# Kernel tuning notes

Hardware: AMD Instinct MI355X
Metric: run time of the kernel (lower is better)

## Reference

```python
import jax, jax.numpy as jnp
import numpy as np
import math

D_MODEL = 1024
NUM_HEADS = 16
HEAD_DIM = D_MODEL // NUM_HEADS


def setup_inputs() -> dict:
    key = jax.random.key(0)
    ks = jax.random.split(key, 9)
    B, T = 4, 2048
    s = 1.0 / math.sqrt(D_MODEL)
    return {
        "x": jax.random.normal(ks[0], (B, T, D_MODEL), dtype=jnp.float32),
        "Wq": jax.random.normal(ks[1], (D_MODEL, D_MODEL), dtype=jnp.float32) * s,
        "bq": jnp.zeros((D_MODEL,), dtype=jnp.float32),
        "Wk": jax.random.normal(ks[2], (D_MODEL, D_MODEL), dtype=jnp.float32) * s,
        "bk": jnp.zeros((D_MODEL,), dtype=jnp.float32),
        "Wv": jax.random.normal(ks[3], (D_MODEL, D_MODEL), dtype=jnp.float32) * s,
        "bv": jnp.zeros((D_MODEL,), dtype=jnp.float32),
        "Wo": jax.random.normal(ks[4], (D_MODEL, D_MODEL), dtype=jnp.float32) * s,
        "bo": jnp.zeros((D_MODEL,), dtype=jnp.float32),
    }


def reference(x, Wq, bq, Wk, bk, Wv, bv, Wo, bo):
    # x: [B, T, D]. Weights stored as [in, out] (torch Linear weight transposed).
    B, T, D = x.shape
    H, Hd = NUM_HEADS, HEAD_DIM

    def heads(w, b):
        # [B,T,D] -> [B,H,T,Hd]
        return (x @ w + b).reshape(B, T, H, Hd).transpose(0, 2, 1, 3)

    q = heads(Wq, bq)
    k = heads(Wk, bk)
    v = heads(Wv, bv)

    scores = jnp.einsum("bhqd,bhkd->bhqk", q, k) / math.sqrt(Hd)
    attn = jax.nn.softmax(scores, axis=-1)  # dropout is identity in eval mode
    ctx = jnp.einsum("bhqk,bhkd->bhqd", attn, v)
    ctx = ctx.transpose(0, 2, 1, 3).reshape(B, T, D)
    return ctx @ Wo + bo
```

## Files before the change

kernel.cpp:

```cpp
#include <hip/hip_runtime.h>
#include <hip/hip_bf16.h>

#define D_MODEL 1024
#define NHEADS  16
#define HD      64
#define BATCH   4
#define SEQ     2048
#define MROWS   (BATCH*SEQ)
#define NKV     (SEQ/64)

typedef __attribute__((ext_vector_type(8))) short bf16x8;
typedef __attribute__((ext_vector_type(4))) float f32x4;
typedef __attribute__((ext_vector_type(16))) float f32x16;
typedef __attribute__((ext_vector_type(2))) float f32x2;
typedef __attribute__((ext_vector_type(4))) unsigned int u32x4;
typedef __attribute__((ext_vector_type(2))) unsigned int u32x2;
#define MFMA16(a,b,c) __builtin_amdgcn_mfma_f32_16x16x32_bf16(a,b,c,0,0,0)
#define MFMA32(a,b,c) __builtin_amdgcn_mfma_f32_32x32x16_bf16(a,b,c,0,0,0)

__device__ __forceinline__ short f2bf(float f) {
    __hip_bfloat16 h = __float2bfloat16(f);
    return *reinterpret_cast<short*>(&h);
}
__device__ __forceinline__ unsigned cvtpk(float a, float b) {
    unsigned r; asm("v_cvt_pk_bf16_f32 %0, %1, %2" : "=v"(r) : "v"(a), "v"(b)); return r;
}
__device__ __forceinline__ float fexp2(float x) {
    float r; asm("v_exp_f32 %0, %1" : "=v"(r) : "v"(x)); return r;
}
__device__ __forceinline__ f32x2 pkadd(f32x2 a, f32x2 b) {
    f32x2 d; asm("v_pk_add_f32 %0, %1, %2" : "=v"(d) : "v"(a), "v"(b)); return d;
}
#define SH2(V,I) __builtin_shufflevector(V, V, I, (I)+1)

typedef const __attribute__((address_space(1))) unsigned char* gas_t;
typedef __attribute__((address_space(3))) unsigned char* las_t;
#define GLD16(gp, lp) __builtin_amdgcn_global_load_lds((gas_t)(gp), (las_t)(lp), 16, 0, 0)

__global__ __launch_bounds__(256) void prep(
    const float* __restrict__ x,
    const float* __restrict__ Wq, const float* __restrict__ Wk,
    const float* __restrict__ Wv, const float* __restrict__ Wo,
    short* __restrict__ xb,
    short* __restrict__ WqT, short* __restrict__ WkT,
    short* __restrict__ WvT, short* __restrict__ WoT)
{
    __shared__ float tile[64][65];
    const int bid = blockIdx.x;
    const int t = threadIdx.x;
    if (bid < 4096) {
        const size_t i = ((size_t)bid * 256 + t) * 8;
        float4 a = *reinterpret_cast<const float4*>(&x[i]);
        float4 b = *reinterpret_cast<const float4*>(&x[i + 4]);
        bf16x8 v;
        v[0]=f2bf(a.x); v[1]=f2bf(a.y); v[2]=f2bf(a.z); v[3]=f2bf(a.w);
        v[4]=f2bf(b.x); v[5]=f2bf(b.y); v[6]=f2bf(b.z); v[7]=f2bf(b.w);
        *reinterpret_cast<bf16x8*>(&xb[i]) = v;
        return;
    }
    const int tt = bid - 4096;
    const int w = tt >> 8;
    const int tl = tt & 255;
    const int bn = (tl & 15) * 64, bk = (tl >> 4) * 64;
    const float* W = (w==0)?Wq:(w==1)?Wk:(w==2)?Wv:Wo;
    short* out     = (w==0)?WqT:(w==1)?WkT:(w==2)?WvT:WoT;
    const int r = t >> 2, c0 = (t & 3) * 16;
    #pragma unroll
    for (int i = 0; i < 16; i += 4) {
        float4 v = *reinterpret_cast<const float4*>(&W[(size_t)(bk + r) * D_MODEL + bn + c0 + i]);
        tile[r][c0+i] = v.x; tile[r][c0+i+1] = v.y; tile[r][c0+i+2] = v.z; tile[r][c0+i+3] = v.w;
    }
    __syncthreads();
    bf16x8 H0, H1;
    #pragma unroll
    for (int i = 0; i < 8; i++) { H0[i] = f2bf(tile[c0 + i][r]); H1[i] = f2bf(tile[c0 + 8 + i][r]); }
    short* hp = &out[(size_t)(bn + r) * D_MODEL + bk + c0];
    *reinterpret_cast<bf16x8*>(hp) = H0;
    *reinterpret_cast<bf16x8*>(hp + 8) = H1;
}

__global__ __launch_bounds__(256) void gemm_qkv(
    const short* __restrict__ A,
    const short* __restrict__ WqT, const short* __restrict__ WkT, const short* __restrict__ WvT,
    const float* __restrict__ bq, const float* __restrict__ bk, const float* __restrict__ bv,
    short* __restrict__ qo, short* __restrict__ ko, short* __restrict__ vo,
    const float qscale)
{
    __shared__ short As[2][128 * 32];
    __shared__ short Bs[2][128 * 32];
    const int tid = threadIdx.x, wave = tid >> 6, lane = tid & 63;
    const int g = lane >> 4, li = lane & 15;
    const int lin = blockIdx.x + blockIdx.y * 24;
    const int swz = (lin & 7) * 192 + (lin >> 3);
    const int bx = swz % 24, by = swz / 24;
    const int which = bx >> 3;
    const int bm = by * 128, bn = (bx & 7) * 128;
    const int wr = wave >> 1, wc = wave & 1;
    const int lrow = lane >> 2, lcol = (lane & 3) * 8;

    const short* BT = (which == 0) ? WqT : (which == 1) ? WkT : WvT;
    const float* bias = (which == 0) ? bq : (which == 1) ? bk : bv;
    short* out = (which == 0) ? qo : (which == 1) ? ko : vo;
    const float scale = (which == 0) ? qscale : 1.0f;

    f32x4 acc[4][4];
    #pragma unroll
    for (int i = 0; i < 4; i++)
        #pragma unroll
        for (int j = 0; j < 4; j++)
            #pragma unroll
            for (int r = 0; r < 4; r++) acc[i][j][r] = 0.f;

#define STAGEG(KS, BUF) do { \
        const int k0_ = (KS) * 32; \
        _Pragma("unroll") \
        for (int c = 0; c < 2; c++) { \
            const int ch = wave + c * 4; \
            const int row = ch * 16 + lrow; \
            GLD16(&A [(size_t)(bm + row) * D_MODEL + k0_ + lcol], &As[BUF][ch * 512]); \
            GLD16(&BT[(size_t)(bn + row) * D_MODEL + k0_ + lcol], &Bs[BUF][ch * 512]); \
        } \
    } while (0)

    STAGEG(0, 0);

    const int NSTEP = D_MODEL / 32;
    for (int ks = 0; ks < NSTEP; ks++) {
        const int cur = ks & 1;
        if (ks + 1 < NSTEP) {
            STAGEG(ks + 1, cur ^ 1);
            asm volatile("s_waitcnt vmcnt(4)" ::: "memory");
        } else {
            asm volatile("s_waitcnt vmcnt(0)" ::: "memory");
        }
        __builtin_amdgcn_s_barrier();
        __builtin_amdgcn_sched_barrier(0);

        bf16x8 af[4], bfr[4];
        #pragma unroll
        for (int mi = 0; mi < 4; mi++) af[mi]  = *reinterpret_cast<const bf16x8*>(&As[cur][(wr * 64 + mi * 16 + li) * 32 + g * 8]);
        #pragma unroll
        for (int ni = 0; ni < 4; ni++) bfr[ni] = *reinterpret_cast<const bf16x8*>(&Bs[cur][(wc * 64 + ni * 16 + li) * 32 + g * 8]);
        #pragma unroll
        for (int mi = 0; mi < 4; mi++)
            #pragma unroll
            for (int ni = 0; ni < 4; ni++)
                acc[mi][ni] = MFMA16(af[mi], bfr[ni], acc[mi][ni]);
        __builtin_amdgcn_s_barrier();
    }
#undef STAGEG

    #pragma unroll
    for (int mi = 0; mi < 4; mi++) {
        #pragma unroll
        for (int r = 0; r < 4; r++) {
            const int m = bm + wr * 64 + mi * 16 + g * 4 + r;
            const int b = m >> 11, t = m & (SEQ - 1);
            #pragma unroll
            for (int ni = 0; ni < 4; ni++) {
                const int n = bn + wc * 64 + ni * 16 + li;
                const float val = (acc[mi][ni][r] + bias[n]) * scale;
                const int h = n >> 6, hd = n & 63;
                const int bh = b * NHEADS + h;
                const short sv = f2bf(val);
                if (which == 0) {
                    out[((size_t)bh * SEQ + t) * HD + hd] = sv;
                } else if (which == 1) {
                    const int kt = t >> 6, trow = t & 63;
                    const int rh = trow >> 5, rl = trow & 31;
                    const int dc = hd >> 4, hh = (hd >> 3) & 1, j = hd & 7;
                    out[((((size_t)bh * NKV + kt) * 8 + dc * 2 + rh) * 64 + hh * 32 + rl) * 8 + j] = sv;
                } else {
                    const int kt = t >> 6, trow = t & 63;
                    const int kb2 = trow >> 4, hh = (trow >> 3) & 1, j = trow & 7;
                    const int vh = hd >> 5, rl = hd & 31;
                    out[((((size_t)bh * NKV + kt) * 8 + kb2 * 2 + vh) * 64 + hh * 32 + rl) * 8 + j] = sv;
                }
            }
        }
    }
}

__global__ __launch_bounds__(256) void gemm_wo(
    const short* __restrict__ A, const short* __restrict__ BT,
    const float* __restrict__ bias, float* __restrict__ out)
{
    __shared__ short As[3][128 * 32];
    __shared__ short Bs[3][128 * 32];
    const int tid = threadIdx.x, wave = tid >> 6, lane = tid & 63;
    const int g = lane >> 4, li = lane & 15;
    const int lin = blockIdx.x + blockIdx.y * 8;
    const int swz = (lin & 7) * 64 + (lin >> 3);
    const int bm = (swz >> 3) * 128, bn = (swz & 7) * 128;
    const int wr = wave >> 1, wc = wave & 1;
    const int lrow = lane >> 2, lcol = (lane & 3) * 8;

    f32x4 acc[4][4];
    #pragma unroll
    for (int i = 0; i < 4; i++)
        #pragma unroll
        for (int j = 0; j < 4; j++)
            #pragma unroll
            for (int r = 0; r < 4; r++) acc[i][j][r] = 0.f;

#define STAGEG(KS, BUF) do { \
        const int k0_ = (KS) * 32; \
        _Pragma("unroll") \
        for (int c = 0; c < 2; c++) { \
            const int ch = wave + c * 4; \
            const int row = ch * 16 + lrow; \
            GLD16(&A [(size_t)(bm + row) * D_MODEL + k0_ + lcol], &As[BUF][ch * 512]); \
            GLD16(&BT[(size_t)(bn + row) * D_MODEL + k0_ + lcol], &Bs[BUF][ch * 512]); \
        } \
    } while (0)

    STAGEG(0, 0);
    STAGEG(1, 1);

    const int NSTEP = D_MODEL / 32;
    for (int ks = 0; ks < NSTEP; ks++) {
        const int cur = ks % 3;
        if (ks + 2 < NSTEP) {
            STAGEG(ks + 2, (ks + 2) % 3);
            asm volatile("s_waitcnt vmcnt(8)" ::: "memory");
        } else if (ks + 1 < NSTEP) {
            asm volatile("s_waitcnt vmcnt(4)" ::: "memory");
        } else {
            asm volatile("s_waitcnt vmcnt(0)" ::: "memory");
        }
        __builtin_amdgcn_s_barrier();
        __builtin_amdgcn_sched_barrier(0);

        bf16x8 af[4], bfr[4];
        #pragma unroll
        for (int mi = 0; mi < 4; mi++) af[mi]  = *reinterpret_cast<const bf16x8*>(&As[cur][(wr * 64 + mi * 16 + li) * 32 + g * 8]);
        #pragma unroll
        for (int ni = 0; ni < 4; ni++) bfr[ni] = *reinterpret_cast<const bf16x8*>(&Bs[cur][(wc * 64 + ni * 16 + li) * 32 + g * 8]);
        #pragma unroll
        for (int mi = 0; mi < 4; mi++)
            #pragma unroll
            for (int ni = 0; ni < 4; ni++)
                acc[mi][ni] = MFMA16(af[mi], bfr[ni], acc[mi][ni]);
        __builtin_amdgcn_s_barrier();
    }
#undef STAGEG

    #pragma unroll
    for (int mi = 0; mi < 4; mi++) {
        #pragma unroll
        for (int r = 0; r < 4; r++) {
            const int m = bm + wr * 64 + mi * 16 + g * 4 + r;
            #pragma unroll
            for (int ni = 0; ni < 4; ni++) {
                const int n = bn + wc * 64 + ni * 16 + li;
                out[(size_t)m * D_MODEL + n] = acc[mi][ni][r] + bias[n];
            }
        }
    }
}

__global__ __launch_bounds__(256) void attn_mfma(
    const short* __restrict__ q, const short* __restrict__ kblk,
    const short* __restrict__ vblk, short* __restrict__ ch)
{
    __shared__ short Ks[2][64 * 64];
    __shared__ short Vs[2][64 * 64];

    const int bh = blockIdx.x;
    const int b  = bh >> 4, h = bh & (NHEADS - 1);
    const int qt = blockIdx.y;
    const int tid = threadIdx.x;
    const int wave = tid >> 6, lane = tid & 63;
    const int ql = lane & 31;
    const int hi = lane >> 5;
    const int lb = lane * 8;

    const short* qp = q + ((size_t)bh * SEQ + qt * 128 + wave * 32 + ql) * HD;
    const bf16x8 qf0 = *reinterpret_cast<const bf16x8*>(qp + 0  + hi * 8);
    const bf16x8 qf1 = *reinterpret_cast<const bf16x8*>(qp + 16 + hi * 8);
    const bf16x8 qf2 = *reinterpret_cast<const bf16x8*>(qp + 32 + hi * 8);
    const bf16x8 qf3 = *reinterpret_cast<const bf16x8*>(qp + 48 + hi * 8);

    f32x16 o0, o1, Z;
    #pragma unroll
    for (int i = 0; i < 16; i++) { o0[i] = 0.f; o1[i] = 0.f; Z[i] = 0.f; }
    float lR = 0.f;

    const int r0 = wave * 2, r1 = wave * 2 + 1;

#define STAGE(T, BUF) do { \
        const short* kg_ = kblk + ((size_t)(bh * NKV + (T)) * 8) * 512; \
        const short* vg_ = vblk + ((size_t)(bh * NKV + (T)) * 8) * 512; \
        GLD16(kg_ + r0 * 512 + lb, &Ks[BUF][r0 * 512]); \
        GLD16(kg_ + r1 * 512 + lb, &Ks[BUF][r1 * 512]); \
        GLD16(vg_ + r0 * 512 + lb, &Vs[BUF][r0 * 512]); \
        GLD16(vg_ + r1 * 512 + lb, &Vs[BUF][r1 * 512]); \
    } while (0)

    u32x4 pp[4];
    bf16x8 vr0[4], vr1[4];

    STAGE(0, 0);

    const int NT = NKV;
    for (int kt = 0; kt < NT; kt++) {
        const int cur = kt & 1;
        if (kt + 1 < NT) {
            STAGE(kt + 1, cur ^ 1);
            asm volatile("s_waitcnt vmcnt(4)" ::: "memory");
        } else {
            asm volatile("s_waitcnt vmcnt(0)" ::: "memory");
        }
        __builtin_amdgcn_s_barrier();
        __builtin_amdgcn_sched_barrier(0);

        const short* Kb = Ks[cur];
        const short* Vb = Vs[cur];

        f32x16 s0, s1;
        __builtin_amdgcn_s_setprio(1);
#define QK_STEP(DC, QF, C0, C1) do { \
            const bf16x8 ka0 = *reinterpret_cast<const bf16x8*>(&Kb[((DC) * 2 + 0) * 512 + lb]); \
            const bf16x8 ka1 = *reinterpret_cast<const bf16x8*>(&Kb[((DC) * 2 + 1) * 512 + lb]); \
            s0 = MFMA32(ka0, QF, C0); \
            s1 = MFMA32(ka1, QF, C1); \
        } while (0)
        QK_STEP(0, qf0, Z, Z);
        QK_STEP(1, qf1, s0, s1);
        QK_STEP(2, qf2, s0, s1);
        QK_STEP(3, qf3, s0, s1);
#undef QK_STEP

        if (kt > 0) {
            #pragma unroll
            for (int KB = 0; KB < 4; KB++) {
                const bf16x8 pf = __builtin_bit_cast(bf16x8, pp[KB]);
                o0 = MFMA32(vr0[KB], pf, o0);
                o1 = MFMA32(vr1[KB], pf, o1);
            }
        }
        #pragma unroll
        for (int KB = 0; KB < 4; KB++) {
            vr0[KB] = *reinterpret_cast<const bf16x8*>(&Vb[(KB * 2 + 0) * 512 + lb]);
            vr1[KB] = *reinterpret_cast<const bf16x8*>(&Vb[(KB * 2 + 1) * 512 + lb]);
        }
        __builtin_amdgcn_s_setprio(0);

        #pragma unroll
        for (int i = 0; i < 16; i++) s0[i] = fexp2(s0[i]);
        #pragma unroll
        for (int i = 0; i < 16; i++) s1[i] = fexp2(s1[i]);
        {
            f32x2 p0 = pkadd(SH2(s0, 0), SH2(s0, 2));
            f32x2 p1 = pkadd(SH2(s0, 4), SH2(s0, 6));
            f32x2 p2 = pkadd(SH2(s0, 8), SH2(s0, 10));
            f32x2 p3 = pkadd(SH2(s0, 12), SH2(s0, 14));
            f32x2 p4 = pkadd(SH2(s1, 0), SH2(s1, 2));
            f32x2 p5 = pkadd(SH2(s1, 4), SH2(s1, 6));
            f32x2 p6 = pkadd(SH2(s1, 8), SH2(s1, 10));
            f32x2 p7 = pkadd(SH2(s1, 12), SH2(s1, 14));
            p0 = pkadd(p0, p1); p2 = pkadd(p2, p3);
            p4 = pkadd(p4, p5); p6 = pkadd(p6, p7);
            p0 = pkadd(p0, p2); p4 = pkadd(p4, p6);
            p0 = pkadd(p0, p4);
            float sum = p0[0] + p0[1];
            sum += __shfl_xor(sum, 32);
            lR += sum;
        }

#define PACK(KB, SS, B) do { \
            const unsigned a0 = cvtpk(SS[(B) + 0], SS[(B) + 1]); \
            const unsigned a1 = cvtpk(SS[(B) + 2], SS[(B) + 3]); \
            const unsigned a2 = cvtpk(SS[(B) + 4], SS[(B) + 5]); \
            const unsigned a3 = cvtpk(SS[(B) + 6], SS[(B) + 7]); \
            const u32x2 r02 = __builtin_amdgcn_permlane32_swap(a0, a2, false, false); \
            const u32x2 r13 = __builtin_amdgcn_permlane32_swap(a1, a3, false, false); \
            pp[KB][0] = r02[0]; pp[KB][1] = r13[0]; pp[KB][2] = r02[1]; pp[KB][3] = r13[1]; \
        } while (0)
        PACK(0, s0, 0); PACK(1, s0, 8); PACK(2, s1, 0); PACK(3, s1, 8);
#undef PACK

        asm volatile("s_waitcnt lgkmcnt(0)" ::: "memory");
        __builtin_amdgcn_sched_barrier(0);
        __builtin_amdgcn_s_barrier();
    }
#undef STAGE

    #pragma unroll
    for (int KB = 0; KB < 4; KB++) {
        const bf16x8 pf = __builtin_bit_cast(bf16x8, pp[KB]);
        o0 = MFMA32(vr0[KB], pf, o0);
        o1 = MFMA32(vr1[KB], pf, o1);
    }

    const float inv = 1.0f / lR;
    const int t = qt * 128 + wave * 32 + ql;
    const size_t base = ((size_t)(b * SEQ + t)) * D_MODEL + h * HD;
    #pragma unroll
    for (int blk = 0; blk < 4; blk++) {
        uint2 w0, w1;
        w0.x = cvtpk(o0[4*blk + 0] * inv, o0[4*blk + 1] * inv);
        w0.y = cvtpk(o0[4*blk + 2] * inv, o0[4*blk + 3] * inv);
        w1.x = cvtpk(o1[4*blk + 0] * inv, o1[4*blk + 1] * inv);
        w1.y = cvtpk(o1[4*blk + 2] * inv, o1[4*blk + 3] * inv);
        *reinterpret_cast<uint2*>(&ch[base + 8*blk + 4*hi])      = w0;
        *reinterpret_cast<uint2*>(&ch[base + 32 + 8*blk + 4*hi]) = w1;
    }
}

extern "C" void kernel_launch(void* const* d_in, const int* in_sizes, int n_in,
                              void* d_out, int out_size, void* d_ws, size_t ws_size,
                              hipStream_t stream) {
    const float* x  = (const float*)d_in[0];
    const float* Wq = (const float*)d_in[1];
    const float* bq = (const float*)d_in[2];
    const float* Wk = (const float*)d_in[3];
    const float* bk = (const float*)d_in[4];
    const float* Wv = (const float*)d_in[5];
    const float* bv = (const float*)d_in[6];
    const float* Wo = (const float*)d_in[7];
    const float* bo = (const float*)d_in[8];

    const size_t S1 = (size_t)MROWS * D_MODEL;
    const size_t SW = (size_t)D_MODEL * D_MODEL;
    short* xb  = (short*)d_ws;
    short* qb  = xb + S1;
    short* kb  = qb + S1;
    short* vb  = kb + S1;
    short* chb = vb + S1;
    short* WqT = chb + S1;
    short* WkT = WqT + SW;
    short* WvT = WkT + SW;
    short* WoT = WvT + SW;

    prep<<<5120, 256, 0, stream>>>(x, Wq, Wk, Wv, Wo, xb, WqT, WkT, WvT, WoT);

    const float QSCALE = 0.125f * 1.4426950408889634f;
    gemm_qkv<<<dim3(24, 64), 256, 0, stream>>>(xb, WqT, WkT, WvT, bq, bk, bv,
                                               qb, kb, vb, QSCALE);
    attn_mfma<<<dim3(BATCH * NHEADS, SEQ / 128), 256, 0, stream>>>(qb, kb, vb, chb);
    gemm_wo<<<dim3(8, 64), 256, 0, stream>>>(chb, WoT, bo, (float*)d_out);
}
```

Measured before the change: 203.9 us.

## Double per-wave query rows in attention and triple-buffer QKV GEMM loads

The attention kernel now gives each wave two 32-row query groups (256 rows per block), so every K/V tile staged into shared memory is reused by twice as many queries. This halves the K/V traffic per query and halves the grid. The P·V step is no longer deferred to the next iteration; it runs right after each half's exp and sum, so one half's softmax can interleave with the other's MFMAs. The QKV GEMM moves from a two-stage to a three-stage LDS pipeline so loads are issued two steps ahead. The costs are more registers and fewer blocks (occupancy, a 512-block grid on many CUs), plus more shared memory in the GEMM.

```diff
diff --git a/kernel.cpp b/kernel.cpp
--- a/kernel.cpp
+++ b/kernel.cpp
@@ -86,8 +86,8 @@
     short* __restrict__ qo, short* __restrict__ ko, short* __restrict__ vo,
     const float qscale)
 {
-    __shared__ short As[2][128 * 32];
-    __shared__ short Bs[2][128 * 32];
+    __shared__ short As[3][128 * 32];
+    __shared__ short Bs[3][128 * 32];
     const int tid = threadIdx.x, wave = tid >> 6, lane = tid & 63;
     const int g = lane >> 4, li = lane & 15;
     const int lin = blockIdx.x + blockIdx.y * 24;
@@ -123,12 +123,15 @@
     } while (0)
 
     STAGEG(0, 0);
+    STAGEG(1, 1);
 
     const int NSTEP = D_MODEL / 32;
     for (int ks = 0; ks < NSTEP; ks++) {
-        const int cur = ks & 1;
-        if (ks + 1 < NSTEP) {
-            STAGEG(ks + 1, cur ^ 1);
+        const int cur = ks % 3;
+        if (ks + 2 < NSTEP) {
+            STAGEG(ks + 2, (ks + 2) % 3);
+            asm volatile("s_waitcnt vmcnt(8)" ::: "memory");
+        } else if (ks + 1 < NSTEP) {
             asm volatile("s_waitcnt vmcnt(4)" ::: "memory");
         } else {
             asm volatile("s_waitcnt vmcnt(0)" ::: "memory");
@@ -275,16 +278,19 @@
     const int hi = lane >> 5;
     const int lb = lane * 8;
 
-    const short* qp = q + ((size_t)bh * SEQ + qt * 128 + wave * 32 + ql) * HD;
-    const bf16x8 qf0 = *reinterpret_cast<const bf16x8*>(qp + 0  + hi * 8);
-    const bf16x8 qf1 = *reinterpret_cast<const bf16x8*>(qp + 16 + hi * 8);
-    const bf16x8 qf2 = *reinterpret_cast<const bf16x8*>(qp + 32 + hi * 8);
-    const bf16x8 qf3 = *reinterpret_cast<const bf16x8*>(qp + 48 + hi * 8);
-
-    f32x16 o0, o1, Z;
-    #pragma unroll
-    for (int i = 0; i < 16; i++) { o0[i] = 0.f; o1[i] = 0.f; Z[i] = 0.f; }
-    float lR = 0.f;
+    const short* qpA = q + ((size_t)bh * SEQ + qt * 256 + wave * 64 + ql) * HD;
+    const short* qpB = qpA + 32 * HD;
+    bf16x8 qfA[4], qfB[4];
+    #pragma unroll
+    for (int dc = 0; dc < 4; dc++) {
+        qfA[dc] = *reinterpret_cast<const bf16x8*>(qpA + dc * 16 + hi * 8);
+        qfB[dc] = *reinterpret_cast<const bf16x8*>(qpB + dc * 16 + hi * 8);
+    }
+
+    f32x16 oA0, oA1, oB0, oB1, Z;
+    #pragma unroll
+    for (int i = 0; i < 16; i++) { oA0[i] = 0.f; oA1[i] = 0.f; oB0[i] = 0.f; oB1[i] = 0.f; Z[i] = 0.f; }
+    float lRA = 0.f, lRB = 0.f;
 
     const int r0 = wave * 2, r1 = wave * 2 + 1;
 
@@ -297,9 +303,6 @@
         GLD16(vg_ + r1 * 512 + lb, &Vs[BUF][r1 * 512]); \
     } while (0)
 
-    u32x4 pp[4];
-    bf16x8 vr0[4], vr1[4];
-
     STAGE(0, 0);
 
     const int NT = NKV;
@@ -317,68 +320,93 @@
         const short* Kb = Ks[cur];
         const short* Vb = Vs[cur];
 
-        f32x16 s0, s1;
+        f32x16 sA0, sA1, sB0, sB1;
         __builtin_amdgcn_s_setprio(1);
-#define QK_STEP(DC, QF, C0, C1) do { \
+#define QK_STEP(DC, CA0, CA1, CB0, CB1) do { \
             const bf16x8 ka0 = *reinterpret_cast<const bf16x8*>(&Kb[((DC) * 2 + 0) * 512 + lb]); \
             const bf16x8 ka1 = *reinterpret_cast<const bf16x8*>(&Kb[((DC) * 2 + 1) * 512 + lb]); \
-            s0 = MFMA32(ka0, QF, C0); \
-            s1 = MFMA32(ka1, QF, C1); \
+            sA0 = MFMA32(ka0, qfA[DC], CA0); \
+            sA1 = MFMA32(ka1, qfA[DC], CA1); \
+            sB0 = MFMA32(ka0, qfB[DC], CB0); \
+            sB1 = MFMA32(ka1, qfB[DC], CB1); \
         } while (0)
-        QK_STEP(0, qf0, Z, Z);
-        QK_STEP(1, qf1, s0, s1);
-        QK_STEP(2, qf2, s0, s1);
-        QK_STEP(3, qf3, s0, s1);
+        QK_STEP(0, Z, Z, Z, Z);
+        QK_STEP(1, sA0, sA1, sB0, sB1);
+        QK_STEP(2, sA0, sA1, sB0, sB1);
+        QK_STEP(3, sA0, sA1, sB0, sB1);
 #undef QK_STEP
-
-        if (kt > 0) {
-            #pragma unroll
-            for (int KB = 0; KB < 4; KB++) {
-                const bf16x8 pf = __builtin_bit_cast(bf16x8, pp[KB]);
-                o0 = MFMA32(vr0[KB], pf, o0);
-                o1 = MFMA32(vr1[KB], pf, o1);
-            }
-        }
-        #pragma unroll
-        for (int KB = 0; KB < 4; KB++) {
-            vr0[KB] = *reinterpret_cast<const bf16x8*>(&Vb[(KB * 2 + 0) * 512 + lb]);
-            vr1[KB] = *reinterpret_cast<const bf16x8*>(&Vb[(KB * 2 + 1) * 512 + lb]);
-        }
         __builtin_amdgcn_s_setprio(0);
 
-        #pragma unroll
-        for (int i = 0; i < 16; i++) s0[i] = fexp2(s0[i]);
-        #pragma unroll
-        for (int i = 0; i < 16; i++) s1[i] = fexp2(s1[i]);
+        bf16x8 vf[8];
+        #pragma unroll
+        for (int rr = 0; rr < 8; rr++)
+            vf[rr] = *reinterpret_cast<const bf16x8*>(&Vb[rr * 512 + lb]);
+
+        #pragma unroll
+        for (int i = 0; i < 16; i++) sA0[i] = fexp2(sA0[i]);
+        #pragma unroll
+        for (int i = 0; i < 16; i++) sA1[i] = fexp2(sA1[i]);
         {
-            f32x2 p0 = pkadd(SH2(s0, 0), SH2(s0, 2));
-            f32x2 p1 = pkadd(SH2(s0, 4), SH2(s0, 6));
-            f32x2 p2 = pkadd(SH2(s0, 8), SH2(s0, 10));
-            f32x2 p3 = pkadd(SH2(s0, 12), SH2(s0, 14));
-            f32x2 p4 = pkadd(SH2(s1, 0), SH2(s1, 2));
-            f32x2 p5 = pkadd(SH2(s1, 4), SH2(s1, 6));
-            f32x2 p6 = pkadd(SH2(s1, 8), SH2(s1, 10));
-            f32x2 p7 = pkadd(SH2(s1, 12), SH2(s1, 14));
+            f32x2 p0 = pkadd(SH2(sA0, 0), SH2(sA0, 2));
+            f32x2 p1 = pkadd(SH2(sA0, 4), SH2(sA0, 6));
+            f32x2 p2 = pkadd(SH2(sA0, 8), SH2(sA0, 10));
+            f32x2 p3 = pkadd(SH2(sA0, 12), SH2(sA0, 14));
+            f32x2 p4 = pkadd(SH2(sA1, 0), SH2(sA1, 2));
+            f32x2 p5 = pkadd(SH2(sA1, 4), SH2(sA1, 6));
+            f32x2 p6 = pkadd(SH2(sA1, 8), SH2(sA1, 10));
+            f32x2 p7 = pkadd(SH2(sA1, 12), SH2(sA1, 14));
             p0 = pkadd(p0, p1); p2 = pkadd(p2, p3);
             p4 = pkadd(p4, p5); p6 = pkadd(p6, p7);
             p0 = pkadd(p0, p2); p4 = pkadd(p4, p6);
             p0 = pkadd(p0, p4);
             float sum = p0[0] + p0[1];
             sum += __shfl_xor(sum, 32);
-            lR += sum;
-        }
-
-#define PACK(KB, SS, B) do { \
+            lRA += sum;
+        }
+        __builtin_amdgcn_s_setprio(1);
+#define PV_STEP(KB, SS, B, O0, O1) do { \
             const unsigned a0 = cvtpk(SS[(B) + 0], SS[(B) + 1]); \
             const unsigned a1 = cvtpk(SS[(B) + 2], SS[(B) + 3]); \
             const unsigned a2 = cvtpk(SS[(B) + 4], SS[(B) + 5]); \
             const unsigned a3 = cvtpk(SS[(B) + 6], SS[(B) + 7]); \
             const u32x2 r02 = __builtin_amdgcn_permlane32_swap(a0, a2, false, false); \
             const u32x2 r13 = __builtin_amdgcn_permlane32_swap(a1, a3, false, false); \
-            pp[KB][0] = r02[0]; pp[KB][1] = r13[0]; pp[KB][2] = r02[1]; pp[KB][3] = r13[1]; \
+            u32x4 wv; \
+            wv[0] = r02[0]; wv[1] = r13[0]; wv[2] = r02[1]; wv[3] = r13[1]; \
+            const bf16x8 pf = __builtin_bit_cast(bf16x8, wv); \
+            O0 = MFMA32(vf[(KB) * 2 + 0], pf, O0); \
+            O1 = MFMA32(vf[(KB) * 2 + 1], pf, O1); \
         } while (0)
-        PACK(0, s0, 0); PACK(1, s0, 8); PACK(2, s1, 0); PACK(3, s1, 8);
-#undef PACK
+        PV_STEP(0, sA0, 0, oA0, oA1); PV_STEP(1, sA0, 8, oA0, oA1);
+        PV_STEP(2, sA1, 0, oA0, oA1); PV_STEP(3, sA1, 8, oA0, oA1);
+        __builtin_amdgcn_s_setprio(0);
+
+        #pragma unroll
+        for (int i = 0; i < 16; i++) sB0[i] = fexp2(sB0[i]);
+        #pragma unroll
+        for (int i = 0; i < 16; i++) sB1[i] = fexp2(sB1[i]);
+        {
+            f32x2 p0 = pkadd(SH2(sB0, 0), SH2(sB0, 2));
+            f32x2 p1 = pkadd(SH2(sB0, 4), SH2(sB0, 6));
+            f32x2 p2 = pkadd(SH2(sB0, 8), SH2(sB0, 10));
+            f32x2 p3 = pkadd(SH2(sB0, 12), SH2(sB0, 14));
+            f32x2 p4 = pkadd(SH2(sB1, 0), SH2(sB1, 2));
+            f32x2 p5 = pkadd(SH2(sB1, 4), SH2(sB1, 6));
+            f32x2 p6 = pkadd(SH2(sB1, 8), SH2(sB1, 10));
+            f32x2 p7 = pkadd(SH2(sB1, 12), SH2(sB1, 14));
+            p0 = pkadd(p0, p1); p2 = pkadd(p2, p3);
+            p4 = pkadd(p4, p5); p6 = pkadd(p6, p7);
+            p0 = pkadd(p0, p2); p4 = pkadd(p4, p6);
+            p0 = pkadd(p0, p4);
+            float sum = p0[0] + p0[1];
+            sum += __shfl_xor(sum, 32);
+            lRB += sum;
+        }
+        __builtin_amdgcn_s_setprio(1);
+        PV_STEP(0, sB0, 0, oB0, oB1); PV_STEP(1, sB0, 8, oB0, oB1);
+        PV_STEP(2, sB1, 0, oB0, oB1); PV_STEP(3, sB1, 8, oB0, oB1);
+#undef PV_STEP
+        __builtin_amdgcn_s_setprio(0);
 
         asm volatile("s_waitcnt lgkmcnt(0)" ::: "memory");
         __builtin_amdgcn_sched_barrier(0);
@@ -386,25 +414,26 @@
     }
 #undef STAGE
 
-    #pragma unroll
-    for (int KB = 0; KB < 4; KB++) {
-        const bf16x8 pf = __builtin_bit_cast(bf16x8, pp[KB]);
-        o0 = MFMA32(vr0[KB], pf, o0);
-        o1 = MFMA32(vr1[KB], pf, o1);
-    }
-
-    const float inv = 1.0f / lR;
-    const int t = qt * 128 + wave * 32 + ql;
-    const size_t base = ((size_t)(b * SEQ + t)) * D_MODEL + h * HD;
+    const int tA = qt * 256 + wave * 64 + ql;
+    const float invA = 1.0f / lRA;
+    const size_t baseA = ((size_t)(b * SEQ + tA)) * D_MODEL + h * HD;
+    const float invB = 1.0f / lRB;
+    const size_t baseB = ((size_t)(b * SEQ + tA + 32)) * D_MODEL + h * HD;
     #pragma unroll
     for (int blk = 0; blk < 4; blk++) {
         uint2 w0, w1;
-        w0.x = cvtpk(o0[4*blk + 0] * inv, o0[4*blk + 1] * inv);
-        w0.y = cvtpk(o0[4*blk + 2] * inv, o0[4*blk + 3] * inv);
-        w1.x = cvtpk(o1[4*blk + 0] * inv, o1[4*blk + 1] * inv);
-        w1.y = cvtpk(o1[4*blk + 2] * inv, o1[4*blk + 3] * inv);
-        *reinterpret_cast<uint2*>(&ch[base + 8*blk + 4*hi])      = w0;
-        *reinterpret_cast<uint2*>(&ch[base + 32 + 8*blk + 4*hi]) = w1;
+        w0.x = cvtpk(oA0[4*blk + 0] * invA, oA0[4*blk + 1] * invA);
+        w0.y = cvtpk(oA0[4*blk + 2] * invA, oA0[4*blk + 3] * invA);
+        w1.x = cvtpk(oA1[4*blk + 0] * invA, oA1[4*blk + 1] * invA);
+        w1.y = cvtpk(oA1[4*blk + 2] * invA, oA1[4*blk + 3] * invA);
+        *reinterpret_cast<uint2*>(&ch[baseA + 8*blk + 4*hi])      = w0;
+        *reinterpret_cast<uint2*>(&ch[baseA + 32 + 8*blk + 4*hi]) = w1;
+        w0.x = cvtpk(oB0[4*blk + 0] * invB, oB0[4*blk + 1] * invB);
+        w0.y = cvtpk(oB0[4*blk + 2] * invB, oB0[4*blk + 3] * invB);
+        w1.x = cvtpk(oB1[4*blk + 0] * invB, oB1[4*blk + 1] * invB);
+        w1.y = cvtpk(oB1[4*blk + 2] * invB, oB1[4*blk + 3] * invB);
+        *reinterpret_cast<uint2*>(&ch[baseB + 8*blk + 4*hi])      = w0;
+        *reinterpret_cast<uint2*>(&ch[baseB + 32 + 8*blk + 4*hi]) = w1;
     }
 }
 
@@ -438,6 +467,6 @@
     const float QSCALE = 0.125f * 1.4426950408889634f;
     gemm_qkv<<<dim3(24, 64), 256, 0, stream>>>(xb, WqT, WkT, WvT, bq, bk, bv,
                                                qb, kb, vb, QSCALE);
-    attn_mfma<<<dim3(BATCH * NHEADS, SEQ / 128), 256, 0, stream>>>(qb, kb, vb, chb);
+    attn_mfma<<<dim3(BATCH * NHEADS, SEQ / 256), 256, 0, stream>>>(qb, kb, vb, chb);
     gemm_wo<<<dim3(8, 64), 256, 0, stream>>>(chb, WoT, bo, (float*)d_out);
 }
```

After: 223.3 us. 1.1x slower.

## Triple-buffer QKV GEMM loads and compute softmax row sums via MFMA

Applied to the files above, without the earlier changes.

The QKV projection GEMM moves from double to triple buffering in LDS, issuing loads two k-steps ahead with adjusted vmcnt waits so more global latency is hidden. The attention kernel drops the per-tile VALU packed-add reduction and cross-lane shuffle for the softmax denominator. It instead accumulates row sums with an extra MFMA against a ones vector, using the bf16-rounded probabilities. This trades VALU work for about 50% more PV MFMA work. It also raises LDS use in the GEMM, which may lower occupancy.

```diff
diff --git a/kernel.cpp b/kernel.cpp
--- a/kernel.cpp
+++ b/kernel.cpp
@@ -28,10 +28,6 @@
 __device__ __forceinline__ float fexp2(float x) {
     float r; asm("v_exp_f32 %0, %1" : "=v"(r) : "v"(x)); return r;
 }
-__device__ __forceinline__ f32x2 pkadd(f32x2 a, f32x2 b) {
-    f32x2 d; asm("v_pk_add_f32 %0, %1, %2" : "=v"(d) : "v"(a), "v"(b)); return d;
-}
-#define SH2(V,I) __builtin_shufflevector(V, V, I, (I)+1)
 
 typedef const __attribute__((address_space(1))) unsigned char* gas_t;
 typedef __attribute__((address_space(3))) unsigned char* las_t;
@@ -86,8 +82,8 @@
     short* __restrict__ qo, short* __restrict__ ko, short* __restrict__ vo,
     const float qscale)
 {
-    __shared__ short As[2][128 * 32];
-    __shared__ short Bs[2][128 * 32];
+    __shared__ short As[3][128 * 32];
+    __shared__ short Bs[3][128 * 32];
     const int tid = threadIdx.x, wave = tid >> 6, lane = tid & 63;
     const int g = lane >> 4, li = lane & 15;
     const int lin = blockIdx.x + blockIdx.y * 24;
@@ -123,12 +119,15 @@
     } while (0)
 
     STAGEG(0, 0);
+    STAGEG(1, 1);
 
     const int NSTEP = D_MODEL / 32;
     for (int ks = 0; ks < NSTEP; ks++) {
-        const int cur = ks & 1;
-        if (ks + 1 < NSTEP) {
-            STAGEG(ks + 1, cur ^ 1);
+        const int cur = ks % 3;
+        if (ks + 2 < NSTEP) {
+            STAGEG(ks + 2, (ks + 2) % 3);
+            asm volatile("s_waitcnt vmcnt(8)" ::: "memory");
+        } else if (ks + 1 < NSTEP) {
             asm volatile("s_waitcnt vmcnt(4)" ::: "memory");
         } else {
             asm volatile("s_waitcnt vmcnt(0)" ::: "memory");
@@ -281,10 +280,13 @@
     const bf16x8 qf2 = *reinterpret_cast<const bf16x8*>(qp + 32 + hi * 8);
     const bf16x8 qf3 = *reinterpret_cast<const bf16x8*>(qp + 48 + hi * 8);
 
-    f32x16 o0, o1, Z;
-    #pragma unroll
-    for (int i = 0; i < 16; i++) { o0[i] = 0.f; o1[i] = 0.f; Z[i] = 0.f; }
-    float lR = 0.f;
+    bf16x8 onesv;
+    #pragma unroll
+    for (int i = 0; i < 8; i++) onesv[i] = (short)0x3F80;
+
+    f32x16 o0, o1, accS, Z;
+    #pragma unroll
+    for (int i = 0; i < 16; i++) { o0[i] = 0.f; o1[i] = 0.f; accS[i] = 0.f; Z[i] = 0.f; }
 
     const int r0 = wave * 2, r1 = wave * 2 + 1;
 
@@ -337,6 +339,7 @@
                 const bf16x8 pf = __builtin_bit_cast(bf16x8, pp[KB]);
                 o0 = MFMA32(vr0[KB], pf, o0);
                 o1 = MFMA32(vr1[KB], pf, o1);
+                accS = MFMA32(onesv, pf, accS);
             }
         }
         #pragma unroll
@@ -350,23 +353,6 @@
         for (int i = 0; i < 16; i++) s0[i] = fexp2(s0[i]);
         #pragma unroll
         for (int i = 0; i < 16; i++) s1[i] = fexp2(s1[i]);
-        {
-            f32x2 p0 = pkadd(SH2(s0, 0), SH2(s0, 2));
-            f32x2 p1 = pkadd(SH2(s0, 4), SH2(s0, 6));
-            f32x2 p2 = pkadd(SH2(s0, 8), SH2(s0, 10));
-            f32x2 p3 = pkadd(SH2(s0, 12), SH2(s0, 14));
-            f32x2 p4 = pkadd(SH2(s1, 0), SH2(s1, 2));
-            f32x2 p5 = pkadd(SH2(s1, 4), SH2(s1, 6));
-            f32x2 p6 = pkadd(SH2(s1, 8), SH2(s1, 10));
-            f32x2 p7 = pkadd(SH2(s1, 12), SH2(s1, 14));
-            p0 = pkadd(p0, p1); p2 = pkadd(p2, p3);
-            p4 = pkadd(p4, p5); p6 = pkadd(p6, p7);
-            p0 = pkadd(p0, p2); p4 = pkadd(p4, p6);
-            p0 = pkadd(p0, p4);
-            float sum = p0[0] + p0[1];
-            sum += __shfl_xor(sum, 32);
-            lR += sum;
-        }
 
 #define PACK(KB, SS, B) do { \
             const unsigned a0 = cvtpk(SS[(B) + 0], SS[(B) + 1]); \
@@ -391,9 +377,10 @@
         const bf16x8 pf = __builtin_bit_cast(bf16x8, pp[KB]);
         o0 = MFMA32(vr0[KB], pf, o0);
         o1 = MFMA32(vr1[KB], pf, o1);
-    }
-
-    const float inv = 1.0f / lR;
+        accS = MFMA32(onesv, pf, accS);
+    }
+
+    const float inv = 1.0f / accS[0];
     const int t = qt * 128 + wave * 32 + ql;
     const size_t base = ((size_t)(b * SEQ + t)) * D_MODEL + h * HD;
     #pragma unroll
```

Result: faster. 199.4 us (-2.2%).
